# Optimization experiments

Measured on AMD Instinct MI355X. Metric: run time of the kernel, lower is better.

Reference implementation:

```python
import jax, jax.numpy as jnp
import numpy as np

N, E, D, H, C, HOPS = 50000, 1600000, 128, 4, 32, 3

def spectral_normalize(W, iters=5):
    # power iteration, fixed start vector (deterministic, jit-friendly)
    u = jnp.ones((W.shape[0],), W.dtype) / jnp.sqrt(jnp.float32(W.shape[0]))
    for _ in range(iters):
        v = W.T @ u; v = v / (jnp.linalg.norm(v) + 1e-12)
        u = W @ v;  u = u / (jnp.linalg.norm(u) + 1e-12)
    sigma = u @ (W @ v)
    return W / (sigma + 1e-12)

def layer_norm(x, g, b, eps=1e-5):
    m = jnp.mean(x, -1, keepdims=True)
    v = jnp.mean((x - m) ** 2, -1, keepdims=True)
    return (x - m) * jax.lax.rsqrt(v + eps) * g + b

def edge_softmax(logits, dst):
    # logits: [E, H]; softmax over edges sharing a destination node
    m = jax.ops.segment_max(logits, dst, num_segments=N)
    e = jnp.exp(logits - m[dst])
    s = jax.ops.segment_sum(e, dst, num_segments=N)
    return e / (s[dst] + 1e-16)

def gat_layer(h, src, dst, W, a_s, a_d, bias):
    xh = (h @ W).reshape(N, H, C)                      # [N,H,C]
    al_s = jnp.sum(xh * a_s, -1)                       # [N,H]
    al_d = jnp.sum(xh * a_d, -1)
    logits = jax.nn.leaky_relu(al_s[src] + al_d[dst], 0.2)  # [E,H]
    alpha = edge_softmax(logits, dst)                  # [E,H]
    msg = xh[src] * alpha[..., None]                   # [E,H,C]
    out = jax.ops.segment_sum(msg, dst, num_segments=N)
    return out.reshape(N, H * C) + bias

def ode_block(h, W_ode, b_ode, steps=4):
    # fixed-step RK4 over t in [0,1]; f(h) = gelu(h @ sn(W) + b)
    Wn = spectral_normalize(W_ode)
    f = lambda y: jax.nn.gelu(y @ Wn + b_ode, approximate=False)
    dt = 1.0 / steps
    def step(y, _):
        k1 = f(y); k2 = f(y + 0.5 * dt * k1)
        k3 = f(y + 0.5 * dt * k2); k4 = f(y + dt * k3)
        return y + (dt / 6.0) * (k1 + 2 * k2 + 2 * k3 + k4), None
    y, _ = jax.lax.scan(step, h, None, length=steps)
    return y

def multihop_broadcast(h, src, dst, att):
    deg = jnp.maximum(jax.ops.segment_sum(jnp.ones((E,), h.dtype), dst, num_segments=N), 1.0)
    hops = [h]
    cur = h
    for _ in range(HOPS):
        cur = jax.ops.segment_sum(cur[src], dst, num_segments=N) / deg[:, None]
        hops.append(cur)
    stack = jnp.stack(hops)                            # [HOPS+1, N, D]
    scores = jnp.einsum('knd,d->kn', stack, att)       # [HOPS+1, N]
    w = jax.nn.softmax(scores, axis=0)
    return jnp.einsum('kn,knd->nd', w, stack)

def encoder_fwd(x, edge_index, W_in, b_in, W1, a_src1, a_dst1, b1,
                W2, a_src2, a_dst2, b2, g1, be1, g2, be2, W_ode, b_ode, att):
    src, dst = edge_index[0], edge_index[1]
    h = jax.nn.gelu(x @ spectral_normalize(W_in) + b_in, approximate=False)
    h = layer_norm(jax.nn.gelu(gat_layer(h, src, dst, W1, a_src1, a_dst1, b1), approximate=False), g1, be1)
    h = layer_norm(jax.nn.gelu(gat_layer(h, src, dst, W2, a_src2, a_dst2, b2), approximate=False), g2, be2)
    h = ode_block(h, W_ode, b_ode)
    h = multihop_broadcast(h, src, dst, att)
    return h

def setup_inputs() -> dict:
    key = jax.random.key(0)
    ks = jax.random.split(key, 12)
    s = lambda d: 1.0 / np.sqrt(d)
    return {
        'x': jax.random.normal(ks[0], (N, D), jnp.float32),
        'edge_index': jax.random.randint(ks[1], (2, E), 0, N, jnp.int64),
        'W_in': jax.random.normal(ks[2], (D, D), jnp.float32) * s(D),
        'b_in': jnp.zeros((D,), jnp.float32),
        'W1': jax.random.normal(ks[3], (D, H * C), jnp.float32) * s(D),
        'a_src1': jax.random.normal(ks[4], (H, C), jnp.float32) * s(C),
        'a_dst1': jax.random.normal(ks[5], (H, C), jnp.float32) * s(C),
        'b1': jnp.zeros((H * C,), jnp.float32),
        'W2': jax.random.normal(ks[6], (D, H * C), jnp.float32) * s(D),
        'a_src2': jax.random.normal(ks[7], (H, C), jnp.float32) * s(C),
        'a_dst2': jax.random.normal(ks[8], (H, C), jnp.float32) * s(C),
        'b2': jnp.zeros((H * C,), jnp.float32),
        'g1': jnp.ones((D,), jnp.float32), 'be1': jnp.zeros((D,), jnp.float32),
        'g2': jnp.ones((D,), jnp.float32), 'be2': jnp.zeros((D,), jnp.float32),
        'W_ode': jax.random.normal(ks[9], (D, D), jnp.float32) * s(D),
        'b_ode': jnp.zeros((D,), jnp.float32),
        'att': jax.random.normal(ks[10], (D,), jnp.float32) * s(D),
    }

def reference(x, edge_index, W_in, b_in, W1, a_src1, a_dst1, b1, W2, a_src2, a_dst2, b2,
              g1, be1, g2, be2, W_ode, b_ode, att):
    return encoder_fwd(x, edge_index, W_in, b_in, W1, a_src1, a_dst1, b1,
                       W2, a_src2, a_dst2, b2, g1, be1, g2, be2, W_ode, b_ode, att)
```

## Files before the change

kernel.cpp:

```cpp
#include <hip/hip_runtime.h>
#include <math.h>


typedef __attribute__((ext_vector_type(8))) short bf16x8;
typedef __attribute__((ext_vector_type(4))) float f32x4;

#define BSN 256

__device__ __forceinline__ float gelu_f(float x) {
    return 0.5f * x * (1.0f + erff(x * 0.70710678118654752f));
}
__device__ __forceinline__ float gelu_fast(float x) {
    float y = 0.7978845608028654f * fmaf(0.044715f * x, x * x, x);
    float e = __expf(-2.0f * y);
    return x / (1.0f + e);
}
__device__ __forceinline__ unsigned pack_bf16(float a, float b) {
    unsigned ua = __float_as_uint(a), ub = __float_as_uint(b);
    ua += 0x7fffu + ((ua >> 16) & 1u);
    ub += 0x7fffu + ((ub >> 16) & 1u);
    return (ua >> 16) | (ub & 0xffff0000u);
}
__device__ __forceinline__ unsigned short bfbits(float x) {
    unsigned u = __float_as_uint(x);
    u += 0x7fffu + ((u >> 16) & 1u);
    return (unsigned short)(u >> 16);
}
__device__ __forceinline__ float bf_lo(unsigned u) { return __uint_as_float(u << 16); }
__device__ __forceinline__ float bf_hi(unsigned u) { return __uint_as_float(u & 0xffff0000u); }
__device__ __forceinline__ int swz(int byte) { return byte ^ (((byte >> 8) & 15) << 4); }

__launch_bounds__(128, 1)
__global__ void sn_k(const float* __restrict__ Win, const float* __restrict__ Wode,
                     float* __restrict__ WnIn, float* __restrict__ WnOde)
{
    __shared__ float Ws[128 * 128];
    __shared__ float Wt[128 * 128];
    __shared__ float red[128];
    const float* W  = (blockIdx.x == 0) ? Win  : Wode;
    float*       Wn = (blockIdx.x == 0) ? WnIn : WnOde;
    const int t = threadIdx.x;

    for (int i = t * 4; i < 16384; i += 512) {
        float4 v = *(const float4*)&W[i];
        *(float4*)&Ws[i] = v;
        int r = i >> 7, c = i & 127;
        Wt[(c + 0) * 128 + r] = v.x;
        Wt[(c + 1) * 128 + r] = v.y;
        Wt[(c + 2) * 128 + r] = v.z;
        Wt[(c + 3) * 128 + r] = v.w;
    }
    __syncthreads();

    float u = 0.088388347648318447f;
    float v = 0.0f;
    for (int it = 0; it < 5; it++) {
        red[t] = u; __syncthreads();
        float vv = 0.f;
        for (int i = 0; i < 128; i++) vv = fmaf(Ws[i * 128 + t], red[i], vv);
        __syncthreads();
        red[t] = vv * vv; __syncthreads();
        for (int s = 64; s > 0; s >>= 1) { if (t < s) red[t] += red[t + s]; __syncthreads(); }
        float nv = sqrtf(red[0]) + 1e-12f;
        v = vv / nv;
        __syncthreads();
        red[t] = v; __syncthreads();
        float uu = 0.f;
        for (int i = 0; i < 128; i++) uu = fmaf(Wt[i * 128 + t], red[i], uu);
        __syncthreads();
        red[t] = uu * uu; __syncthreads();
        for (int s = 64; s > 0; s >>= 1) { if (t < s) red[t] += red[t + s]; __syncthreads(); }
        float nu = sqrtf(red[0]) + 1e-12f;
        u = uu / nu;
        __syncthreads();
    }
    red[t] = v; __syncthreads();
    float wv = 0.f;
    for (int i = 0; i < 128; i++) wv = fmaf(Wt[i * 128 + t], red[i], wv);
    __syncthreads();
    red[t] = u * wv; __syncthreads();
    for (int s = 64; s > 0; s >>= 1) { if (t < s) red[t] += red[t + s]; __syncthreads(); }
    float inv = 1.0f / (red[0] + 1e-12f);
    __syncthreads();
    for (int i = t * 4; i < 16384; i += 512) {
        float4 w = *(const float4*)&Ws[i];
        w.x *= inv; w.y *= inv; w.z *= inv; w.w *= inv;
        *(float4*)&Wn[i] = w;
    }
}

__global__ void hist_k(const int* __restrict__ dst, int* __restrict__ deg, int E, int N)
{
    int e = blockIdx.x * blockDim.x + threadIdx.x;
    if (e < E) {
        int d = dst[e];
        d = (d < 0) ? 0 : (d >= N ? N - 1 : d);
        atomicAdd(&deg[d], 1);
    }
}

__launch_bounds__(1024, 1)
__global__ void scan_k(const int* __restrict__ deg, int* __restrict__ offs, int n)
{
    __shared__ int part[1024];
    const int t = threadIdx.x;
    const int chunk = (n + 1023) >> 10;
    int lo = t * chunk; if (lo > n) lo = n;
    int hi = lo + chunk; if (hi > n) hi = n;
    int s = 0;
    for (int i = lo; i < hi; i++) s += deg[i];
    part[t] = s; __syncthreads();
    for (int d = 1; d < 1024; d <<= 1) {
        int v = (t >= d) ? part[t - d] : 0;
        __syncthreads();
        part[t] += v;
        __syncthreads();
    }
    int run = (t == 0) ? 0 : part[t - 1];
    for (int i = lo; i < hi; i++) { offs[i] = run; run += deg[i]; }
    if (t == 1023) offs[n] = run;
}

__global__ void binit_k(const int* __restrict__ offs, int* __restrict__ bcur, int N, int nb)
{
    int b = blockIdx.x * blockDim.x + threadIdx.x;
    if (b < nb) {
        int n = b * BSN; if (n > N) n = N;
        bcur[b] = offs[n];
    }
}

__launch_bounds__(256, 2)
__global__ void scatA_k(const int* __restrict__ src, const int* __restrict__ dst,
                        int* __restrict__ bcur, uint2* __restrict__ pairbuf, int E, int N)
{
    __shared__ int cnt[256];
    __shared__ int sc[256];
    __shared__ int ebase[256];
    __shared__ int delta[256];
    __shared__ uint2 pr[4096];
    __shared__ unsigned char bid[4096];
    const int t = threadIdx.x;
    const int e0 = blockIdx.x * 4096;

    int s[16], d[16], rk[16], bb[16];
    cnt[t] = 0;
    __syncthreads();
#pragma unroll
    for (int i = 0; i < 16; i++) {
        int e = e0 + i * 256 + t;
        if (e < E) {
            int dd = dst[e]; dd = (dd < 0) ? 0 : (dd >= N ? N - 1 : dd);
            int ss = src[e]; ss = (ss < 0) ? 0 : (ss >= N ? N - 1 : ss);
            s[i] = ss; d[i] = dd; bb[i] = dd >> 8;
            rk[i] = atomicAdd(&cnt[bb[i]], 1);
        } else bb[i] = -1;
    }
    __syncthreads();
    sc[t] = cnt[t]; __syncthreads();
    for (int st = 1; st < 256; st <<= 1) {
        int v = (t >= st) ? sc[t - st] : 0;
        __syncthreads();
        sc[t] += v;
        __syncthreads();
    }
    int excl = sc[t] - cnt[t];
    int gbase = (cnt[t] > 0) ? atomicAdd(&bcur[t], cnt[t]) : 0;
    ebase[t] = excl;
    delta[t] = gbase - excl;
    __syncthreads();
#pragma unroll
    for (int i = 0; i < 16; i++) {
        if (bb[i] >= 0) {
            int slot = ebase[bb[i]] + rk[i];
            pr[slot] = make_uint2((unsigned)s[i], (unsigned)d[i]);
            bid[slot] = (unsigned char)bb[i];
        }
    }
    __syncthreads();
    const int total = sc[255];
    for (int i2 = t; i2 < total; i2 += 256) {
        int b = bid[i2];
        pairbuf[delta[b] + i2] = pr[i2];
    }
}

__launch_bounds__(256, 4)
__global__ void scatB_k(const uint2* __restrict__ pairbuf, const int* __restrict__ offs,
                        int* __restrict__ col, int N)
{
    __shared__ int cur[BSN];
    const int b = blockIdx.x;
    const int n0 = b * BSN;
    const int t = threadIdx.x;
    int nn = N - n0; if (nn > BSN) nn = BSN;
    if (t < nn) cur[t] = offs[n0 + t];
    __syncthreads();
    const int es = offs[n0], ee = offs[n0 + nn];
    for (int e = es + t; e < ee; e += 256) {
        uint2 p = pairbuf[e];
        int pos = atomicAdd(&cur[(int)p.y - n0], 1);
        col[pos] = (int)p.x;
    }
}

__launch_bounds__(256, 2)
__global__ void gemm_mfma_k(const float* __restrict__ in, const float* __restrict__ W,
                            const float* __restrict__ bias, float* __restrict__ out_f32,
                            unsigned short* __restrict__ out_bf, int nrows, int mode,
                            const float* __restrict__ a_s, const float* __restrict__ a_d,
                            float* __restrict__ als, float* __restrict__ ald)
{
    __shared__ unsigned short Wt[128 * 128];
    __shared__ unsigned short As[128 * 128];
    const int t = threadIdx.x;
    const int w = t >> 6, lane = t & 63;
    const int cl = lane & 15, lg = lane >> 4;
    const int r0 = blockIdx.x * 128;

    for (int i = t; i < 16384; i += 256) {
        int k = i >> 7, c = i & 127;
        *(unsigned short*)((char*)Wt + swz((c << 8) + (k << 1))) = bfbits(W[i]);
    }
    for (int i2 = t; i2 < 4096; i2 += 256) {
        int r = i2 >> 5, k0 = (i2 & 31) * 4;
        int rc = r0 + r; if (rc > nrows - 1) rc = nrows - 1;
        float4 v = *(const float4*)&in[(size_t)rc * 128 + k0];
        *(uint2*)((char*)As + swz((r << 8) + (k0 << 1))) =
            make_uint2(pack_bf16(v.x, v.y), pack_bf16(v.z, v.w));
    }
    __syncthreads();

    bf16x8 af[2][4];
#pragma unroll
    for (int rt = 0; rt < 2; rt++)
#pragma unroll
        for (int ks = 0; ks < 4; ks++)
            af[rt][ks] = *(const bf16x8*)((char*)As +
                           swz((w * 32 + rt * 16 + cl) * 256 + ks * 64 + lg * 16));

    f32x4 acc[2][8];
#pragma unroll
    for (int rt = 0; rt < 2; rt++)
#pragma unroll
        for (int n = 0; n < 8; n++) acc[rt][n] = (f32x4){0.f, 0.f, 0.f, 0.f};

#pragma unroll
    for (int n = 0; n < 8; n++) {
#pragma unroll
        for (int ks = 0; ks < 4; ks++) {
            bf16x8 bf = *(const bf16x8*)((char*)Wt +
                          swz((n * 16 + cl) * 256 + ks * 64 + lg * 16));
            acc[0][n] = __builtin_amdgcn_mfma_f32_16x16x32_bf16(af[0][ks], bf, acc[0][n], 0, 0, 0);
            acc[1][n] = __builtin_amdgcn_mfma_f32_16x16x32_bf16(af[1][ks], bf, acc[1][n], 0, 0, 0);
        }
    }

    if (mode == 0) {
        float asv[4][2], adv[4][2];
#pragma unroll
        for (int h = 0; h < 4; h++) {
            asv[h][0] = a_s[h * 32 + cl];      asv[h][1] = a_s[h * 32 + 16 + cl];
            adv[h][0] = a_d[h * 32 + cl];      adv[h][1] = a_d[h * 32 + 16 + cl];
        }
#pragma unroll
        for (int rt = 0; rt < 2; rt++) {
#pragma unroll
            for (int q = 0; q < 4; q++) {
                int row = r0 + w * 32 + rt * 16 + lg * 4 + q;
                float sh[4], dh[4];
#pragma unroll
                for (int h = 0; h < 4; h++) {
                    sh[h] = acc[rt][2 * h][q] * asv[h][0] + acc[rt][2 * h + 1][q] * asv[h][1];
                    dh[h] = acc[rt][2 * h][q] * adv[h][0] + acc[rt][2 * h + 1][q] * adv[h][1];
                }
#pragma unroll
                for (int mk = 1; mk < 16; mk <<= 1) {
#pragma unroll
                    for (int h = 0; h < 4; h++) {
                        sh[h] += __shfl_xor(sh[h], mk);
                        dh[h] += __shfl_xor(dh[h], mk);
                    }
                }
                if (cl == 0 && row < nrows) {
#pragma unroll
                    for (int h = 0; h < 4; h++) {
                        als[(size_t)row * 4 + h] = sh[h];
                        ald[(size_t)row * 4 + h] = dh[h];
                    }
                }
            }
#pragma unroll
            for (int q = 0; q < 4; q++) {
                int row = r0 + w * 32 + rt * 16 + lg * 4 + q;
                if (row < nrows) {
#pragma unroll
                    for (int n = 0; n < 8; n++)
                        out_bf[(size_t)row * 128 + n * 16 + cl] = bfbits(acc[rt][n][q]);
                }
            }
        }
    } else {
        float bc[8];
#pragma unroll
        for (int n = 0; n < 8; n++) bc[n] = bias[n * 16 + cl];
#pragma unroll
        for (int rt = 0; rt < 2; rt++)
#pragma unroll
            for (int q = 0; q < 4; q++) {
                int row = r0 + w * 32 + rt * 16 + lg * 4 + q;
                if (row < nrows) {
#pragma unroll
                    for (int n = 0; n < 8; n++)
                        out_f32[(size_t)row * 128 + n * 16 + cl] =
                            gelu_f(acc[rt][n][q] + bc[n]);
                }
            }
    }
}

__launch_bounds__(256)
__global__ void gat_agg2_k(const unsigned* __restrict__ xhbf, const float* __restrict__ als,
                           const float* __restrict__ ald, const int* __restrict__ col,
                           const int* __restrict__ offs, const float* __restrict__ bias,
                           const float* __restrict__ g, const float* __restrict__ be,
                           float* __restrict__ hout, int nnodes)
{
    __shared__ float alph[8][32][4];
    __shared__ int   scol[8][32];
    const int gq = threadIdx.x >> 5;
    const int n = blockIdx.x * 8 + gq;
    if (n >= nnodes) return;
    const int l = threadIdx.x & 31;
    const int e0 = offs[n], e1 = offs[n + 1];
    const float4 aldv = *(const float4*)&ald[(size_t)n * 4];

    float m0 = -1e30f, m1 = -1e30f, m2 = -1e30f, m3 = -1e30f;
    float s0 = 0.f, s1 = 0.f, s2 = 0.f, s3 = 0.f;
    for (int i = e0 + l; i < e1; i += 32) {
        int sv = col[i];
        float4 av = *(const float4*)&als[(size_t)sv * 4];
        float l0 = av.x + aldv.x; l0 = l0 > 0.f ? l0 : 0.2f * l0;
        float l1 = av.y + aldv.y; l1 = l1 > 0.f ? l1 : 0.2f * l1;
        float l2 = av.z + aldv.z; l2 = l2 > 0.f ? l2 : 0.2f * l2;
        float l3 = av.w + aldv.w; l3 = l3 > 0.f ? l3 : 0.2f * l3;
        float M;
        M = fmaxf(m0, l0); s0 = s0 * __expf(m0 - M) + __expf(l0 - M); m0 = M;
        M = fmaxf(m1, l1); s1 = s1 * __expf(m1 - M) + __expf(l1 - M); m1 = M;
        M = fmaxf(m2, l2); s2 = s2 * __expf(m2 - M) + __expf(l2 - M); m2 = M;
        M = fmaxf(m3, l3); s3 = s3 * __expf(m3 - M) + __expf(l3 - M); m3 = M;
    }
#pragma unroll
    for (int mk = 1; mk < 32; mk <<= 1) {
        float mo, so, M;
        mo = __shfl_xor(m0, mk); so = __shfl_xor(s0, mk);
        M = fmaxf(m0, mo); s0 = s0 * __expf(m0 - M) + so * __expf(mo - M); m0 = M;
        mo = __shfl_xor(m1, mk); so = __shfl_xor(s1, mk);
        M = fmaxf(m1, mo); s1 = s1 * __expf(m1 - M) + so * __expf(mo - M); m1 = M;
        mo = __shfl_xor(m2, mk); so = __shfl_xor(s2, mk);
        M = fmaxf(m2, mo); s2 = s2 * __expf(m2 - M) + so * __expf(mo - M); m2 = M;
        mo = __shfl_xor(m3, mk); so = __shfl_xor(s3, mk);
        M = fmaxf(m3, mo); s3 = s3 * __expf(m3 - M) + so * __expf(mo - M); m3 = M;
    }
    const float i0 = 1.f / (s0 + 1e-16f), i1 = 1.f / (s1 + 1e-16f);
    const float i2 = 1.f / (s2 + 1e-16f), i3 = 1.f / (s3 + 1e-16f);

    const int hh = l >> 3;
    float a0 = 0.f, a1 = 0.f, a2 = 0.f, a3 = 0.f;
    for (int base = e0; base < e1; base += 32) {
        int idx = base + l;
        if (idx < e1) {
            int sv = col[idx];
            float4 av = *(const float4*)&als[(size_t)sv * 4];
            float l0 = av.x + aldv.x; l0 = l0 > 0.f ? l0 : 0.2f * l0;
            float l1 = av.y + aldv.y; l1 = l1 > 0.f ? l1 : 0.2f * l1;
            float l2 = av.z + aldv.z; l2 = l2 > 0.f ? l2 : 0.2f * l2;
            float l3 = av.w + aldv.w; l3 = l3 > 0.f ? l3 : 0.2f * l3;
            float4 a4;
            a4.x = __expf(l0 - m0) * i0;
            a4.y = __expf(l1 - m1) * i1;
            a4.z = __expf(l2 - m2) * i2;
            a4.w = __expf(l3 - m3) * i3;
            *(float4*)&alph[gq][l][0] = a4;
            scol[gq][l] = sv;
        }
        int cnt = e1 - base; if (cnt > 32) cnt = 32;
#pragma unroll 4
        for (int j = 0; j < cnt; j++) {
            int sj = scol[gq][j];
            float aj = alph[gq][j][hh];
            uint2 u = *(const uint2*)&xhbf[(size_t)sj * 64 + l * 2];
            a0 = fmaf(aj, bf_lo(u.x), a0);
            a1 = fmaf(aj, bf_hi(u.x), a1);
            a2 = fmaf(aj, bf_lo(u.y), a2);
            a3 = fmaf(aj, bf_hi(u.y), a3);
        }
    }

    const int c0 = l * 4;
    float4 bv = *(const float4*)&bias[c0];
    float v0 = gelu_f(a0 + bv.x);
    float v1 = gelu_f(a1 + bv.y);
    float v2 = gelu_f(a2 + bv.z);
    float v3 = gelu_f(a3 + bv.w);
    float sum = v0 + v1 + v2 + v3;
#pragma unroll
    for (int mk = 1; mk < 32; mk <<= 1) sum += __shfl_xor(sum, mk);
    float mean = sum * (1.0f / 128.0f);
    float d0 = v0 - mean, d1 = v1 - mean, d2 = v2 - mean, d3 = v3 - mean;
    float vs = d0 * d0 + d1 * d1 + d2 * d2 + d3 * d3;
#pragma unroll
    for (int mk = 1; mk < 32; mk <<= 1) vs += __shfl_xor(vs, mk);
    float rstd = rsqrtf(vs * (1.0f / 128.0f) + 1e-5f);
    float4 gv = *(const float4*)&g[c0];
    float4 ev = *(const float4*)&be[c0];
    float4 o;
    o.x = d0 * rstd * gv.x + ev.x;
    o.y = d1 * rstd * gv.y + ev.y;
    o.z = d2 * rstd * gv.z + ev.z;
    o.w = d3 * rstd * gv.w + ev.w;
    *(float4*)&hout[(size_t)n * 128 + c0] = o;
}

__launch_bounds__(256, 4)
__global__ void ode_mfma_k(const float* __restrict__ yin, const float* __restrict__ Wn,
                           const float* __restrict__ bias, unsigned short* __restrict__ ybf,
                           int nrows, int nchunks)
{
    __shared__ unsigned short Wt[128 * 128];
    __shared__ unsigned short tl[2][16 * 128];
    const int t = threadIdx.x;
    const int w = t >> 6, lane = t & 63;
    const int pair = w >> 1, hf = w & 1;
    const int cl = lane & 15, lg = lane >> 4;

    for (int i = t; i < 16384; i += 256) {
        int k = i >> 7, c = i & 127;
        *(unsigned short*)((char*)Wt + swz((c << 8) + (k << 1))) = bfbits(Wn[i]);
    }

    float bcol[4];
#pragma unroll
    for (int n = 0; n < 4; n++) bcol[n] = bias[(hf * 4 + n) * 16 + cl];

    const float dt = 0.25f;
    char* tbase = (char*)&tl[pair][0];

    int chunk = blockIdx.x * 2 + pair;
    if (chunk > nchunks - 1) chunk = nchunks - 1;
    const int r0 = chunk * 16;

    for (int i2 = hf * 64 + lane; i2 < 512; i2 += 128) {
        int r = i2 >> 5, k0 = (i2 & 31) * 4;
        int rc = r0 + r; if (rc > nrows - 1) rc = nrows - 1;
        float4 v = *(const float4*)&yin[(size_t)rc * 128 + k0];
        *(uint2*)(tbase + swz(r * 256 + k0 * 2)) =
            make_uint2(pack_bf16(v.x, v.y), pack_bf16(v.z, v.w));
    }
    float yv[4][4], av[4][4];
#pragma unroll
    for (int q = 0; q < 4; q++) {
        int rc = r0 + lg * 4 + q; if (rc > nrows - 1) rc = nrows - 1;
        const float* rp = &yin[(size_t)rc * 128 + hf * 64 + cl];
#pragma unroll
        for (int n = 0; n < 4; n++) { yv[n][q] = rp[n * 16]; av[n][q] = yv[n][q]; }
    }
    __syncthreads();

#pragma unroll 1
    for (int step = 0; step < 4; step++) {
#pragma unroll 1
        for (int st = 0; st < 4; st++) {
            const float ca = (st == 0 || st == 3) ? dt / 6.f : dt / 3.f;
            const float ct = (st < 2) ? dt * 0.5f : dt;
            const bool last = (st == 3);
            bf16x8 af[4];
#pragma unroll
            for (int ks = 0; ks < 4; ks++)
                af[ks] = *(const bf16x8*)(tbase + swz(cl * 256 + ks * 64 + lg * 16));
            f32x4 acc[4];
#pragma unroll
            for (int n = 0; n < 4; n++) {
                acc[n] = (f32x4){0.f, 0.f, 0.f, 0.f};
#pragma unroll
                for (int ks = 0; ks < 4; ks++) {
                    bf16x8 bf = *(const bf16x8*)((char*)Wt +
                                  swz(((hf * 4 + n) * 16 + cl) * 256 + ks * 64 + lg * 16));
                    acc[n] = __builtin_amdgcn_mfma_f32_16x16x32_bf16(af[ks], bf, acc[n], 0, 0, 0);
                }
            }
            __syncthreads();
#pragma unroll
            for (int n = 0; n < 4; n++) {
#pragma unroll
                for (int q = 0; q < 4; q++) {
                    float kk = gelu_fast(acc[n][q] + bcol[n]);
                    av[n][q] = fmaf(ca, kk, av[n][q]);
                    float tn;
                    if (last) { yv[n][q] = av[n][q]; tn = av[n][q]; }
                    else      { tn = fmaf(ct, kk, yv[n][q]); }
                    int rr = lg * 4 + q;
                    *(unsigned short*)(tbase +
                        swz(rr * 256 + ((hf * 4 + n) * 16 + cl) * 2)) = bfbits(tn);
                }
            }
            __syncthreads();
        }
    }
#pragma unroll
    for (int q = 0; q < 4; q++) {
        int rg = r0 + lg * 4 + q;
        if (rg < nrows) {
#pragma unroll
            for (int n = 0; n < 4; n++)
                ybf[(size_t)rg * 128 + hf * 64 + n * 16 + cl] = bfbits(av[n][q]);
        }
    }
}

__launch_bounds__(256)
__global__ void hop_k(const unsigned* __restrict__ cur, const int* __restrict__ col,
                      const int* __restrict__ offs, const int* __restrict__ deg,
                      unsigned* __restrict__ outbf, int nnodes)
{
    __shared__ int scol[8][32];
    const int gq = threadIdx.x >> 5;
    const int n = blockIdx.x * 8 + gq;
    if (n >= nnodes) return;
    const int l = threadIdx.x & 31;
    const int e0 = offs[n], e1 = offs[n + 1];
    float a0 = 0.f, a1 = 0.f, a2 = 0.f, a3 = 0.f;
    for (int base = e0; base < e1; base += 32) {
        int idx = base + l;
        if (idx < e1) scol[gq][l] = col[idx];
        int cnt = e1 - base; if (cnt > 32) cnt = 32;
#pragma unroll 4
        for (int j = 0; j < cnt; j++) {
            int sj = scol[gq][j];
            uint2 u = *(const uint2*)&cur[(size_t)sj * 64 + l * 2];
            a0 += bf_lo(u.x); a1 += bf_hi(u.x);
            a2 += bf_lo(u.y); a3 += bf_hi(u.y);
        }
    }
    float inv = 1.0f / fmaxf((float)deg[n], 1.0f);
    *(uint2*)&outbf[(size_t)n * 64 + l * 2] =
        make_uint2(pack_bf16(a0 * inv, a1 * inv), pack_bf16(a2 * inv, a3 * inv));
}

__launch_bounds__(256)
__global__ void final2_k(const unsigned* __restrict__ s0b, const unsigned* __restrict__ s1b,
                         const unsigned* __restrict__ s2b, const unsigned* __restrict__ s3b,
                         const float* __restrict__ att, float* __restrict__ outp, int nnodes)
{
    const int n = blockIdx.x * 4 + (threadIdx.x >> 6);
    if (n >= nnodes) return;
    const int lane = threadIdx.x & 63;
    size_t b = (size_t)n * 64 + lane;
    float2 a = *(const float2*)&att[lane * 2];
    unsigned u0 = s0b[b], u1 = s1b[b], u2 = s2b[b], u3 = s3b[b];
    float p0 = bf_lo(u0) * a.x + bf_hi(u0) * a.y;
    float p1 = bf_lo(u1) * a.x + bf_hi(u1) * a.y;
    float p2 = bf_lo(u2) * a.x + bf_hi(u2) * a.y;
    float p3 = bf_lo(u3) * a.x + bf_hi(u3) * a.y;
#pragma unroll
    for (int mk = 32; mk >= 1; mk >>= 1) {
        p0 += __shfl_xor(p0, mk); p1 += __shfl_xor(p1, mk);
        p2 += __shfl_xor(p2, mk); p3 += __shfl_xor(p3, mk);
    }
    float mm = fmaxf(fmaxf(p0, p1), fmaxf(p2, p3));
    float e0 = __expf(p0 - mm), e1 = __expf(p1 - mm), e2 = __expf(p2 - mm), e3 = __expf(p3 - mm);
    float inv = 1.0f / (e0 + e1 + e2 + e3);
    float w0 = e0 * inv, w1 = e1 * inv, w2 = e2 * inv, w3 = e3 * inv;
    float ox = w0 * bf_lo(u0) + w1 * bf_lo(u1) + w2 * bf_lo(u2) + w3 * bf_lo(u3);
    float oy = w0 * bf_hi(u0) + w1 * bf_hi(u1) + w2 * bf_hi(u2) + w3 * bf_hi(u3);
    *(float2*)&outp[(size_t)n * 128 + lane * 2] = make_float2(ox, oy);
}

extern "C" void kernel_launch(void* const* d_in, const int* in_sizes, int n_in,
                              void* d_out, int out_size, void* d_ws, size_t ws_size,
                              hipStream_t stream)
{
    const float* x     = (const float*)d_in[0];
    const int*   ei    = (const int*)d_in[1];
    const float* W_in  = (const float*)d_in[2];
    const float* b_in  = (const float*)d_in[3];
    const float* W1    = (const float*)d_in[4];
    const float* a_s1  = (const float*)d_in[5];
    const float* a_d1  = (const float*)d_in[6];
    const float* b1    = (const float*)d_in[7];
    const float* W2    = (const float*)d_in[8];
    const float* a_s2  = (const float*)d_in[9];
    const float* a_d2  = (const float*)d_in[10];
    const float* b2    = (const float*)d_in[11];
    const float* g1    = (const float*)d_in[12];
    const float* be1   = (const float*)d_in[13];
    const float* g2    = (const float*)d_in[14];
    const float* be2   = (const float*)d_in[15];
    const float* W_ode = (const float*)d_in[16];
    const float* b_ode = (const float*)d_in[17];
    const float* att   = (const float*)d_in[18];

    const int N = in_sizes[0] / 128;
    const int E = in_sizes[1] / 2;
    const int* srcv = ei;
    const int* dstv = ei + E;
    const int nb = (N + BSN - 1) / BSN;

    char* wsb = (char*)d_ws;
    size_t off = 0;
    auto alloc = [&](size_t bytes) -> void* {
        void* p = wsb + off;
        off = (off + bytes + 511) & ~(size_t)511;
        return p;
    };
    float*    WnIn   = (float*)alloc(65536);
    float*    WnOde  = (float*)alloc(65536);
    float*    als    = (float*)alloc((size_t)N * 4 * 4);
    float*    ald    = (float*)alloc((size_t)N * 4 * 4);
    int*      deg    = (int*)alloc((size_t)N * 4);
    int*      bcur   = (int*)alloc((size_t)(nb + 1) * 4);
    int*      offs   = (int*)alloc((size_t)(N + 1) * 4);
    int*      col    = (int*)alloc((size_t)E * 4);
    float*    B0     = (float*)alloc((size_t)N * 128 * 4);
    unsigned* xhbf   = (unsigned*)alloc((size_t)N * 64 * 4);
    unsigned* ybf    = (unsigned*)alloc((size_t)N * 64 * 4);
    unsigned* h2bf   = (unsigned*)alloc((size_t)N * 64 * 4);
    unsigned* h3bf   = (unsigned*)alloc((size_t)N * 64 * 4);
    uint2*    pairbuf = (uint2*)ybf;

    (void)hipMemsetAsync(deg, 0, (size_t)N * 4, stream);

    sn_k<<<2, 128, 0, stream>>>(W_in, W_ode, WnIn, WnOde);
    hist_k<<<(E + 255) / 256, 256, 0, stream>>>(dstv, deg, E, N);
    scan_k<<<1, 1024, 0, stream>>>(deg, offs, N);
    binit_k<<<(nb + 255) / 256, 256, 0, stream>>>(offs, bcur, N, nb);
    scatA_k<<<(E + 4095) / 4096, 256, 0, stream>>>(srcv, dstv, bcur, pairbuf, E, N);
    scatB_k<<<nb, 256, 0, stream>>>(pairbuf, offs, col, N);

    const int gblocks = (N + 127) / 128;
    const int ablocks = (N + 7) / 8;
    const int fblocks = (N + 3) / 4;

    gemm_mfma_k<<<gblocks, 256, 0, stream>>>(x, WnIn, b_in, B0, nullptr, N, 1,
        nullptr, nullptr, nullptr, nullptr);

    gemm_mfma_k<<<gblocks, 256, 0, stream>>>(B0, W1, nullptr, nullptr,
        (unsigned short*)xhbf, N, 0, a_s1, a_d1, als, ald);
    gat_agg2_k<<<ablocks, 256, 0, stream>>>(xhbf, als, ald, col, offs, b1, g1, be1, B0, N);

    gemm_mfma_k<<<gblocks, 256, 0, stream>>>(B0, W2, nullptr, nullptr,
        (unsigned short*)xhbf, N, 0, a_s2, a_d2, als, ald);
    gat_agg2_k<<<ablocks, 256, 0, stream>>>(xhbf, als, ald, col, offs, b2, g2, be2, B0, N);

    const int nchunks = (N + 15) / 16;
    const int oblocks = (nchunks + 1) / 2;
    ode_mfma_k<<<oblocks, 256, 0, stream>>>(B0, WnOde, b_ode, (unsigned short*)ybf, N, nchunks);

    hop_k<<<ablocks, 256, 0, stream>>>(ybf,  col, offs, deg, xhbf, N);
    hop_k<<<ablocks, 256, 0, stream>>>(xhbf, col, offs, deg, h2bf, N);
    hop_k<<<ablocks, 256, 0, stream>>>(h2bf, col, offs, deg, h3bf, N);
    final2_k<<<fblocks, 256, 0, stream>>>(ybf, xhbf, h2bf, h3bf, att, (float*)d_out, N);
}
```

Baseline: 675.7 us.

## Split hop gather into feature quarters and double-buffer ODE stage tile

The multihop gather kernel is restructured so each block handles one quarter of the feature columns for 16 nodes. Each 16-lane group then reads 64 bytes per neighbour row instead of 256, with the intent of improving L2 locality across the quarter-blocks. The cost is that each node's column indices are read four times. The ODE RK4 kernel now double-buffers its LDS stage tile so one __syncthreads per stage can be dropped, precomputes its swizzled LDS addresses, and replaces the GELU division with a hardware reciprocal.

```diff
diff --git a/kernel.cpp b/kernel.cpp
--- a/kernel.cpp
+++ b/kernel.cpp
@@ -10,10 +10,10 @@
 __device__ __forceinline__ float gelu_f(float x) {
     return 0.5f * x * (1.0f + erff(x * 0.70710678118654752f));
 }
-__device__ __forceinline__ float gelu_fast(float x) {
+__device__ __forceinline__ float gelu_sig(float x) {
     float y = 0.7978845608028654f * fmaf(0.044715f * x, x * x, x);
     float e = __expf(-2.0f * y);
-    return x / (1.0f + e);
+    return x * __builtin_amdgcn_rcpf(1.0f + e);
 }
 __device__ __forceinline__ unsigned pack_bf16(float a, float b) {
     unsigned ua = __float_as_uint(a), ub = __float_as_uint(b);
@@ -428,7 +428,7 @@
                            int nrows, int nchunks)
 {
     __shared__ unsigned short Wt[128 * 128];
-    __shared__ unsigned short tl[2][16 * 128];
+    __shared__ unsigned short tl[2][2][16 * 128];
     const int t = threadIdx.x;
     const int w = t >> 6, lane = t & 63;
     const int pair = w >> 1, hf = w & 1;
@@ -443,8 +443,21 @@
 #pragma unroll
     for (int n = 0; n < 4; n++) bcol[n] = bias[(hf * 4 + n) * 16 + cl];
 
+    int radr[4], badr[4], wadr[4][4];
+#pragma unroll
+    for (int ks = 0; ks < 4; ks++)
+        radr[ks] = swz(cl * 256 + ks * 64 + lg * 16);
+#pragma unroll
+    for (int n = 0; n < 4; n++) {
+        badr[n] = swz(((hf * 4 + n) * 16 + cl) * 256);
+#pragma unroll
+        for (int q = 0; q < 4; q++)
+            wadr[n][q] = swz((lg * 4 + q) * 256 + ((hf * 4 + n) * 16 + cl) * 2);
+    }
+
     const float dt = 0.25f;
-    char* tbase = (char*)&tl[pair][0];
+    char* tb0 = (char*)&tl[pair][0][0];
+    char* tb1 = (char*)&tl[pair][1][0];
 
     int chunk = blockIdx.x * 2 + pair;
     if (chunk > nchunks - 1) chunk = nchunks - 1;
@@ -454,7 +467,7 @@
         int r = i2 >> 5, k0 = (i2 & 31) * 4;
         int rc = r0 + r; if (rc > nrows - 1) rc = nrows - 1;
         float4 v = *(const float4*)&yin[(size_t)rc * 128 + k0];
-        *(uint2*)(tbase + swz(r * 256 + k0 * 2)) =
+        *(uint2*)(tb0 + swz(r * 256 + k0 * 2)) =
             make_uint2(pack_bf16(v.x, v.y), pack_bf16(v.z, v.w));
     }
     float yv[4][4], av[4][4];
@@ -467,6 +480,8 @@
     }
     __syncthreads();
 
+    char* pc = tb0;
+    char* pn = tb1;
 #pragma unroll 1
     for (int step = 0; step < 4; step++) {
 #pragma unroll 1
@@ -477,7 +492,7 @@
             bf16x8 af[4];
 #pragma unroll
             for (int ks = 0; ks < 4; ks++)
-                af[ks] = *(const bf16x8*)(tbase + swz(cl * 256 + ks * 64 + lg * 16));
+                af[ks] = *(const bf16x8*)(pc + radr[ks]);
             f32x4 acc[4];
 #pragma unroll
             for (int n = 0; n < 4; n++) {
@@ -485,26 +500,24 @@
 #pragma unroll
                 for (int ks = 0; ks < 4; ks++) {
                     bf16x8 bf = *(const bf16x8*)((char*)Wt +
-                                  swz(((hf * 4 + n) * 16 + cl) * 256 + ks * 64 + lg * 16));
+                                  (badr[n] ^ (((ks * 64 + lg * 16) >> 0))) );
                     acc[n] = __builtin_amdgcn_mfma_f32_16x16x32_bf16(af[ks], bf, acc[n], 0, 0, 0);
                 }
             }
-            __syncthreads();
 #pragma unroll
             for (int n = 0; n < 4; n++) {
 #pragma unroll
                 for (int q = 0; q < 4; q++) {
-                    float kk = gelu_fast(acc[n][q] + bcol[n]);
+                    float kk = gelu_sig(acc[n][q] + bcol[n]);
                     av[n][q] = fmaf(ca, kk, av[n][q]);
                     float tn;
                     if (last) { yv[n][q] = av[n][q]; tn = av[n][q]; }
                     else      { tn = fmaf(ct, kk, yv[n][q]); }
-                    int rr = lg * 4 + q;
-                    *(unsigned short*)(tbase +
-                        swz(rr * 256 + ((hf * 4 + n) * 16 + cl) * 2)) = bfbits(tn);
+                    *(unsigned short*)(pn + wadr[n][q]) = bfbits(tn);
                 }
             }
             __syncthreads();
+            char* tmp = pc; pc = pn; pn = tmp;
         }
     }
 #pragma unroll
@@ -519,32 +532,32 @@
 }
 
 __launch_bounds__(256)
-__global__ void hop_k(const unsigned* __restrict__ cur, const int* __restrict__ col,
-                      const int* __restrict__ offs, const int* __restrict__ deg,
-                      unsigned* __restrict__ outbf, int nnodes)
-{
-    __shared__ int scol[8][32];
-    const int gq = threadIdx.x >> 5;
-    const int n = blockIdx.x * 8 + gq;
+__global__ void hopq_k(const unsigned* __restrict__ cur, const int* __restrict__ col,
+                       const int* __restrict__ offs, const int* __restrict__ deg,
+                       unsigned* __restrict__ outbf, int nnodes, int nbq)
+{
+    __shared__ int scol[16][16];
+    const int qb = blockIdx.x / nbq;
+    const int nb = blockIdx.x - qb * nbq;
+    const int gq = threadIdx.x >> 4;
+    const int n = nb * 16 + gq;
     if (n >= nnodes) return;
-    const int l = threadIdx.x & 31;
+    const int l = threadIdx.x & 15;
     const int e0 = offs[n], e1 = offs[n + 1];
-    float a0 = 0.f, a1 = 0.f, a2 = 0.f, a3 = 0.f;
-    for (int base = e0; base < e1; base += 32) {
+    const unsigned* __restrict__ tbl = cur + qb * 16 + l;
+    float a0 = 0.f, a1 = 0.f;
+    for (int base = e0; base < e1; base += 16) {
         int idx = base + l;
         if (idx < e1) scol[gq][l] = col[idx];
-        int cnt = e1 - base; if (cnt > 32) cnt = 32;
-#pragma unroll 4
+        int cnt = e1 - base; if (cnt > 16) cnt = 16;
+#pragma unroll 8
         for (int j = 0; j < cnt; j++) {
-            int sj = scol[gq][j];
-            uint2 u = *(const uint2*)&cur[(size_t)sj * 64 + l * 2];
-            a0 += bf_lo(u.x); a1 += bf_hi(u.x);
-            a2 += bf_lo(u.y); a3 += bf_hi(u.y);
+            unsigned u = tbl[(size_t)scol[gq][j] * 64];
+            a0 += bf_lo(u); a1 += bf_hi(u);
         }
     }
     float inv = 1.0f / fmaxf((float)deg[n], 1.0f);
-    *(uint2*)&outbf[(size_t)n * 64 + l * 2] =
-        make_uint2(pack_bf16(a0 * inv, a1 * inv), pack_bf16(a2 * inv, a3 * inv));
+    outbf[(size_t)n * 64 + qb * 16 + l] = pack_bf16(a0 * inv, a1 * inv);
 }
 
 __launch_bounds__(256)
@@ -656,8 +669,9 @@
     const int oblocks = (nchunks + 1) / 2;
     ode_mfma_k<<<oblocks, 256, 0, stream>>>(B0, WnOde, b_ode, (unsigned short*)ybf, N, nchunks);
 
-    hop_k<<<ablocks, 256, 0, stream>>>(ybf,  col, offs, deg, xhbf, N);
-    hop_k<<<ablocks, 256, 0, stream>>>(xhbf, col, offs, deg, h2bf, N);
-    hop_k<<<ablocks, 256, 0, stream>>>(h2bf, col, offs, deg, h3bf, N);
+    const int nbq = (N + 15) / 16;
+    hopq_k<<<nbq * 4, 256, 0, stream>>>(ybf,  col, offs, deg, xhbf, N, nbq);
+    hopq_k<<<nbq * 4, 256, 0, stream>>>(xhbf, col, offs, deg, h2bf, N, nbq);
+    hopq_k<<<nbq * 4, 256, 0, stream>>>(h2bf, col, offs, deg, h3bf, N, nbq);
     final2_k<<<fblocks, 256, 0, stream>>>(ybf, xhbf, h2bf, h3bf, att, (float*)d_out, N);
 }
```

Result: slower. 733.0 us (+8.5%).

## Double-buffer ODE stage tiles, widen blocks to 512 threads, precompute LDS addresses

Applied to the files above, without the earlier changes.

The ODE RK4 kernel now ping-pongs between two LDS tile buffers per row chunk, which removes one of the two block barriers per RK stage. Blocks grow to 512 threads covering four 16-row chunks, so each staged copy of the weight matrix is shared by more rows. Swizzled LDS addresses are computed once up front, and the gelu division becomes a hardware reciprocal. The cost is more LDS per block, fewer blocks per CU, and slightly lower precision in the gelu.

```diff
diff --git a/kernel.cpp b/kernel.cpp
--- a/kernel.cpp
+++ b/kernel.cpp
@@ -10,10 +10,10 @@
 __device__ __forceinline__ float gelu_f(float x) {
     return 0.5f * x * (1.0f + erff(x * 0.70710678118654752f));
 }
-__device__ __forceinline__ float gelu_fast(float x) {
+__device__ __forceinline__ float gelu_sig(float x) {
     float y = 0.7978845608028654f * fmaf(0.044715f * x, x * x, x);
     float e = __expf(-2.0f * y);
-    return x / (1.0f + e);
+    return x * __builtin_amdgcn_rcpf(1.0f + e);
 }
 __device__ __forceinline__ unsigned pack_bf16(float a, float b) {
     unsigned ua = __float_as_uint(a), ub = __float_as_uint(b);
@@ -422,19 +422,19 @@
     *(float4*)&hout[(size_t)n * 128 + c0] = o;
 }
 
-__launch_bounds__(256, 4)
+__launch_bounds__(512, 2)
 __global__ void ode_mfma_k(const float* __restrict__ yin, const float* __restrict__ Wn,
                            const float* __restrict__ bias, unsigned short* __restrict__ ybf,
                            int nrows, int nchunks)
 {
     __shared__ unsigned short Wt[128 * 128];
-    __shared__ unsigned short tl[2][16 * 128];
+    __shared__ unsigned short tl[4][2][16 * 128];
     const int t = threadIdx.x;
     const int w = t >> 6, lane = t & 63;
     const int pair = w >> 1, hf = w & 1;
     const int cl = lane & 15, lg = lane >> 4;
 
-    for (int i = t; i < 16384; i += 256) {
+    for (int i = t; i < 16384; i += 512) {
         int k = i >> 7, c = i & 127;
         *(unsigned short*)((char*)Wt + swz((c << 8) + (k << 1))) = bfbits(Wn[i]);
     }
@@ -443,10 +443,25 @@
 #pragma unroll
     for (int n = 0; n < 4; n++) bcol[n] = bias[(hf * 4 + n) * 16 + cl];
 
+    int radr[4], badr[4][4], wadr[4][4];
+#pragma unroll
+    for (int ks = 0; ks < 4; ks++)
+        radr[ks] = swz(cl * 256 + ks * 64 + lg * 16);
+#pragma unroll
+    for (int n = 0; n < 4; n++) {
+#pragma unroll
+        for (int ks = 0; ks < 4; ks++)
+            badr[n][ks] = swz(((hf * 4 + n) * 16 + cl) * 256 + ks * 64 + lg * 16);
+#pragma unroll
+        for (int q = 0; q < 4; q++)
+            wadr[n][q] = swz((lg * 4 + q) * 256 + ((hf * 4 + n) * 16 + cl) * 2);
+    }
+
     const float dt = 0.25f;
-    char* tbase = (char*)&tl[pair][0];
-
-    int chunk = blockIdx.x * 2 + pair;
+    char* tb0 = (char*)&tl[pair][0][0];
+    char* tb1 = (char*)&tl[pair][1][0];
+
+    int chunk = blockIdx.x * 4 + pair;
     if (chunk > nchunks - 1) chunk = nchunks - 1;
     const int r0 = chunk * 16;
 
@@ -454,7 +469,7 @@
         int r = i2 >> 5, k0 = (i2 & 31) * 4;
         int rc = r0 + r; if (rc > nrows - 1) rc = nrows - 1;
         float4 v = *(const float4*)&yin[(size_t)rc * 128 + k0];
-        *(uint2*)(tbase + swz(r * 256 + k0 * 2)) =
+        *(uint2*)(tb0 + swz(r * 256 + k0 * 2)) =
             make_uint2(pack_bf16(v.x, v.y), pack_bf16(v.z, v.w));
     }
     float yv[4][4], av[4][4];
@@ -467,6 +482,8 @@
     }
     __syncthreads();
 
+    char* pc = tb0;
+    char* pn = tb1;
 #pragma unroll 1
     for (int step = 0; step < 4; step++) {
 #pragma unroll 1
@@ -477,34 +494,31 @@
             bf16x8 af[4];
 #pragma unroll
             for (int ks = 0; ks < 4; ks++)
-                af[ks] = *(const bf16x8*)(tbase + swz(cl * 256 + ks * 64 + lg * 16));
+                af[ks] = *(const bf16x8*)(pc + radr[ks]);
             f32x4 acc[4];
 #pragma unroll
             for (int n = 0; n < 4; n++) {
                 acc[n] = (f32x4){0.f, 0.f, 0.f, 0.f};
 #pragma unroll
                 for (int ks = 0; ks < 4; ks++) {
-                    bf16x8 bf = *(const bf16x8*)((char*)Wt +
-                                  swz(((hf * 4 + n) * 16 + cl) * 256 + ks * 64 + lg * 16));
+                    bf16x8 bf = *(const bf16x8*)((char*)Wt + badr[n][ks]);
                     acc[n] = __builtin_amdgcn_mfma_f32_16x16x32_bf16(af[ks], bf, acc[n], 0, 0, 0);
                 }
             }
-            __syncthreads();
 #pragma unroll
             for (int n = 0; n < 4; n++) {
 #pragma unroll
                 for (int q = 0; q < 4; q++) {
-                    float kk = gelu_fast(acc[n][q] + bcol[n]);
+                    float kk = gelu_sig(acc[n][q] + bcol[n]);
                     av[n][q] = fmaf(ca, kk, av[n][q]);
                     float tn;
                     if (last) { yv[n][q] = av[n][q]; tn = av[n][q]; }
                     else      { tn = fmaf(ct, kk, yv[n][q]); }
-                    int rr = lg * 4 + q;
-                    *(unsigned short*)(tbase +
-                        swz(rr * 256 + ((hf * 4 + n) * 16 + cl) * 2)) = bfbits(tn);
+                    *(unsigned short*)(pn + wadr[n][q]) = bfbits(tn);
                 }
             }
             __syncthreads();
+            char* tmp = pc; pc = pn; pn = tmp;
         }
     }
 #pragma unroll
@@ -653,8 +667,8 @@
     gat_agg2_k<<<ablocks, 256, 0, stream>>>(xhbf, als, ald, col, offs, b2, g2, be2, B0, N);
 
     const int nchunks = (N + 15) / 16;
-    const int oblocks = (nchunks + 1) / 2;
-    ode_mfma_k<<<oblocks, 256, 0, stream>>>(B0, WnOde, b_ode, (unsigned short*)ybf, N, nchunks);
+    const int oblocks = (nchunks + 3) / 4;
+    ode_mfma_k<<<oblocks, 512, 0, stream>>>(B0, WnOde, b_ode, (unsigned short*)ybf, N, nchunks);
 
     hop_k<<<ablocks, 256, 0, stream>>>(ybf,  col, offs, deg, xhbf, N);
     hop_k<<<ablocks, 256, 0, stream>>>(xhbf, col, offs, deg, h2bf, N);
```

Result: no change. 663.7 us (-1.8%).
